# Kernel tuning notes

Measured on AMD Instinct MI355X. Metric: run time of the kernel, lower is better.

## Reference

```python
import jax, jax.numpy as jnp
import numpy as np

SPATIAL_SHAPES = ((80, 80), (40, 40), (20, 20))  # strides 8/16/32 on 640x640
NUM_HEADS = 8
N_POINTS = 4
D_MODEL = 256
OFFSET_SCALE = 0.5
N_LEVELS = len(SPATIAL_SHAPES)
TOTAL_P = N_LEVELS * N_POINTS


def setup_inputs() -> dict:
    key = jax.random.key(0)
    ks = jax.random.split(key, 11)
    B, Q = 32, 300
    S = sum(h * w for h, w in SPATIAL_SHAPES)  # 8400
    d = D_MODEL
    s = 0.02
    return {
        "hidden_states": jax.random.normal(ks[0], (B, Q, d), jnp.float32),
        "encoder_hidden_states": jax.random.normal(ks[1], (B, S, d), jnp.float32),
        "reference_points": jax.random.uniform(ks[2], (B, Q, 1, 4), jnp.float32, 0.1, 0.9),
        "W_off": jax.random.normal(ks[3], (d, NUM_HEADS * TOTAL_P * 2), jnp.float32) * s,
        "b_off": jax.random.normal(ks[4], (NUM_HEADS * TOTAL_P * 2,), jnp.float32) * s,
        "W_attn": jax.random.normal(ks[5], (d, NUM_HEADS * TOTAL_P), jnp.float32) * s,
        "b_attn": jax.random.normal(ks[6], (NUM_HEADS * TOTAL_P,), jnp.float32) * s,
        "W_val": jax.random.normal(ks[7], (d, d), jnp.float32) * s,
        "b_val": jax.random.normal(ks[8], (d,), jnp.float32) * s,
        "W_out": jax.random.normal(ks[9], (d, d), jnp.float32) * s,
        "b_out": jax.random.normal(ks[10], (d,), jnp.float32) * s,
    }


def _bilinear_sample(img, grid):
    # img: (N, H, W, C); grid: (N, Q, P, 2), normalized coords in [-1, 1]
    # torch grid_sample(mode='bilinear', padding_mode='zeros', align_corners=False)
    N, Hh, Ww, C = img.shape
    gx = (grid[..., 0] + 1.0) * (Ww * 0.5) - 0.5
    gy = (grid[..., 1] + 1.0) * (Hh * 0.5) - 0.5
    x0 = jnp.floor(gx)
    y0 = jnp.floor(gy)
    wx1 = gx - x0
    wx0 = 1.0 - wx1
    wy1 = gy - y0
    wy0 = 1.0 - wy1
    n_idx = jnp.arange(N)[:, None, None]

    def tap(ix, iy, w):
        valid = (ix >= 0) & (ix < Ww) & (iy >= 0) & (iy < Hh)
        ixc = jnp.clip(ix, 0, Ww - 1).astype(jnp.int32)
        iyc = jnp.clip(iy, 0, Hh - 1).astype(jnp.int32)
        v = img[n_idx, iyc, ixc]  # (N, Q, P, C)
        return v * (w * valid.astype(w.dtype))[..., None]

    return (tap(x0, y0, wx0 * wy0) + tap(x0 + 1.0, y0, wx1 * wy0)
            + tap(x0, y0 + 1.0, wx0 * wy1) + tap(x0 + 1.0, y0 + 1.0, wx1 * wy1))


def reference(hidden_states, encoder_hidden_states, reference_points,
              W_off, b_off, W_attn, b_attn, W_val, b_val, W_out, b_out):
    B, Q, d = hidden_states.shape
    S = encoder_hidden_states.shape[1]
    H = NUM_HEADS
    C = d // H

    value = (encoder_hidden_states @ W_val + b_val).reshape(B, S, H, C)
    offs = (hidden_states @ W_off + b_off).reshape(B, Q, H, TOTAL_P, 2)
    attn = jax.nn.softmax((hidden_states @ W_attn + b_attn).reshape(B, Q, H, TOTAL_P), axis=-1)

    # 4-d reference points branch (boxes): loc = ref_xy + off * (1/P) * ref_wh * offset_scale
    n_points_scale = jnp.full((TOTAL_P, 1), 1.0 / N_POINTS, hidden_states.dtype)
    loc = (reference_points[:, :, None, :, :2]
           + offs * n_points_scale * reference_points[:, :, None, :, 2:] * OFFSET_SCALE)
    grids = 2.0 * loc - 1.0  # method='default'
    grids = grids.transpose(0, 2, 1, 3, 4).reshape(B * H, Q, TOTAL_P, 2)

    value_bh = value.transpose(0, 2, 1, 3).reshape(B * H, S, C)

    samples = []
    start = 0
    p0 = 0
    for (h, w) in SPATIAL_SHAPES:
        v_l = value_bh[:, start:start + h * w].reshape(B * H, h, w, C)
        g_l = grids[:, :, p0:p0 + N_POINTS]
        samples.append(_bilinear_sample(v_l, g_l))
        start += h * w
        p0 += N_POINTS
    sampled = jnp.concatenate(samples, axis=2)  # (B*H, Q, TOTAL_P, C)

    attn_bh = attn.transpose(0, 2, 1, 3).reshape(B * H, Q, TOTAL_P)
    out = jnp.einsum("nqpc,nqp->nqc", sampled, attn_bh)  # (B*H, Q, C)
    out = out.reshape(B, H, Q, C).transpose(0, 2, 1, 3).reshape(B, Q, H * C)
    return out @ W_out + b_out
```

## Files before the change

kernel.cpp:

```cpp
#include <hip/hip_runtime.h>
#include <hip/hip_fp16.h>

#define DEVI __device__ __forceinline__

typedef _Float16 f16x8 __attribute__((ext_vector_type(8)));
typedef float f32x4 __attribute__((ext_vector_type(4)));

static DEVI unsigned short f2h_u(float f) {
    _Float16 h = (_Float16)f;
    return __builtin_bit_cast(unsigned short, h);
}
static DEVI float h2f_u(unsigned short u) {
    return (float)__builtin_bit_cast(_Float16, u);
}
static DEVI unsigned pk2(float a, float b) {
    return (unsigned)f2h_u(a) | ((unsigned)f2h_u(b) << 16);
}


__global__ __launch_bounds__(256) void prep_weights(
    const float* __restrict__ W_val, const float* __restrict__ W_off,
    const float* __restrict__ W_attn, const float* __restrict__ W_out,
    const float* __restrict__ b_off, const float* __restrict__ b_attn,
    unsigned short* __restrict__ Wst, unsigned short* __restrict__ Wct,
    unsigned short* __restrict__ Wot, float* __restrict__ cbias)
{
    int idx = blockIdx.x * 256 + threadIdx.x;
    if (idx < 65536) {
        int n = idx >> 8, k = idx & 255;
        Wst[(((n >> 7) * 32 + (k >> 3)) * 128 + (n & 127)) * 8 + (k & 7)] =
            f2h_u(W_val[k * 256 + n]);
    } else if (idx < 65536 + 73728) {
        int j = idx - 65536;
        int n = j >> 8, k = j & 255;
        Wct[j] = f2h_u(n < 192 ? W_off[k * 192 + n] : W_attn[k * 96 + (n - 192)]);
    } else if (idx < 204800) {
        int j = idx - 139264;
        int n = j >> 8, k = j & 255;
        Wot[j] = f2h_u(W_out[k * 256 + n]);
    } else if (idx < 205088) {
        int j = idx - 204800;
        cbias[j] = (j < 192) ? b_off[j] : b_attn[j - 192];
    }
}

__global__ __launch_bounds__(256, 2) void gemm_value(
    const float* __restrict__ A, const unsigned short* __restrict__ Wst,
    const float* __restrict__ bias, unsigned short* __restrict__ out)
{
    __shared__ __align__(16) unsigned short Bs[32 * 128 * 8];
    const int tid  = threadIdx.x;
    const int wave = tid >> 6;
    const int lane = tid & 63;
    const int l15  = lane & 15;
    const int qd   = lane >> 4;
    const size_t m0 = (size_t)blockIdx.x * 64;

#pragma unroll
    for (int it = 0; it < 16; ++it) {
        const int c = wave * 16 + it;
        const unsigned short* gp = Wst + c * 512 + lane * 8;
        unsigned short* lp = Bs + c * 512;
        __builtin_amdgcn_global_load_lds(
            (const __attribute__((address_space(1))) void*)gp,
            (__attribute__((address_space(3))) void*)lp, 16, 0, 0);
    }

    const float* arow = A + (m0 + wave * 16 + l15) * 256 + qd * 8;
    float4 a0[8], a1[8];
#pragma unroll
    for (int kt = 0; kt < 8; ++kt) {
        a0[kt] = *(const float4*)(arow + kt * 32);
        a1[kt] = *(const float4*)(arow + kt * 32 + 4);
    }
    f16x8 af[8];
#pragma unroll
    for (int kt = 0; kt < 8; ++kt) {
        union { f16x8 v; uint4 u; } t;
        t.u.x = pk2(a0[kt].x, a0[kt].y);
        t.u.y = pk2(a0[kt].z, a0[kt].w);
        t.u.z = pk2(a1[kt].x, a1[kt].y);
        t.u.w = pk2(a1[kt].z, a1[kt].w);
        af[kt] = t.v;
    }

    f32x4 acc[2][8];
#pragma unroll
    for (int h = 0; h < 2; ++h)
#pragma unroll
        for (int i = 0; i < 8; ++i) acc[h][i] = (f32x4){0.f, 0.f, 0.f, 0.f};

    __syncthreads();

#pragma unroll
    for (int kt = 0; kt < 8; ++kt) {
#pragma unroll
        for (int ni = 0; ni < 8; ++ni) {
            f16x8 bf = *(const f16x8*)&Bs[(((kt * 4 + qd) * 128) + ni * 16 + l15) * 8];
            acc[0][ni] = __builtin_amdgcn_mfma_f32_16x16x32_f16(af[kt], bf, acc[0][ni], 0, 0, 0);
        }
    }
    __syncthreads();

#pragma unroll
    for (int it = 0; it < 16; ++it) {
        const int c = wave * 16 + it;
        const unsigned short* gp = Wst + 32768 + c * 512 + lane * 8;
        unsigned short* lp = Bs + c * 512;
        __builtin_amdgcn_global_load_lds(
            (const __attribute__((address_space(1))) void*)gp,
            (__attribute__((address_space(3))) void*)lp, 16, 0, 0);
    }
    __syncthreads();
#pragma unroll
    for (int kt = 0; kt < 8; ++kt) {
#pragma unroll
        for (int ni = 0; ni < 8; ++ni) {
            f16x8 bf = *(const f16x8*)&Bs[(((kt * 4 + qd) * 128) + ni * 16 + l15) * 8];
            acc[1][ni] = __builtin_amdgcn_mfma_f32_16x16x32_f16(af[kt], bf, acc[1][ni], 0, 0, 0);
        }
    }

    constexpr int LDH = 136;
#pragma unroll
    for (int h = 0; h < 2; ++h) {
        __syncthreads();
        unsigned short* Ch = Bs;
#pragma unroll
        for (int ni = 0; ni < 8; ++ni) {
            const float bb = bias[h * 128 + ni * 16 + l15];
#pragma unroll
            for (int r = 0; r < 4; ++r) {
                Ch[(wave * 16 + qd * 4 + r) * LDH + ni * 16 + l15] =
                    f2h_u(acc[h][ni][r] + bb);
            }
        }
        __syncthreads();
        for (int f = tid; f < 64 * 16; f += 256) {
            int row = f >> 4, c8 = f & 15;
            uint4 v = *(uint4*)&Ch[row * LDH + c8 * 8];
            *(uint4*)(out + (m0 + row) * 256 + h * 128 + c8 * 8) = v;
        }
    }
}

template<int BN>
__global__ __launch_bounds__(256) void gemm_f16(
    const float* __restrict__ A, const unsigned short* __restrict__ Wt,
    const float* __restrict__ bias, float* __restrict__ outp, int ldo)
{
    constexpr int NI  = BN / 16;
    constexpr int LDA = 40;
    constexpr int LDB = 40;
    constexpr int LDC = BN + 4;
    constexpr int SM1 = 64 * LDA * 2 + BN * LDB * 2;
    constexpr int SM2 = 64 * LDC * 4;
    constexpr int SMEM = SM1 > SM2 ? SM1 : SM2;
    __shared__ __align__(16) char smem[SMEM];
    unsigned short* As = (unsigned short*)smem;
    unsigned short* Bs = (unsigned short*)(smem + 64 * LDA * 2);
    float* Cs = (float*)smem;

    const int tid  = threadIdx.x;
    const int wave = tid >> 6;
    const int lane = tid & 63;
    const int l15  = lane & 15;
    const int qd   = lane >> 4;
    const int m0   = blockIdx.y * 64;
    const int n0   = blockIdx.x * BN;

    f32x4 acc[NI];
#pragma unroll
    for (int i = 0; i < NI; i++) acc[i] = (f32x4){0.f, 0.f, 0.f, 0.f};

#pragma unroll
    for (int kt = 0; kt < 8; kt++) {
#pragma unroll
        for (int i = 0; i < 2; i++) {
            int f = tid + i * 256;
            int row = f >> 3, c4 = f & 7;
            const float4 v = *(const float4*)(A + (size_t)(m0 + row) * 256 + kt * 32 + c4 * 4);
            uint2 p;
            p.x = pk2(v.x, v.y);
            p.y = pk2(v.z, v.w);
            *(uint2*)&As[row * LDA + c4 * 4] = p;
        }
        for (int f = tid; f < BN * 4; f += 256) {
            int row = f >> 2, ch = f & 3;
            uint4 v = *(const uint4*)(Wt + (size_t)(n0 + row) * 256 + kt * 32 + ch * 8);
            *(uint4*)&Bs[row * LDB + ch * 8] = v;
        }
        __syncthreads();
        f16x8 afr = *(const f16x8*)&As[(wave * 16 + l15) * LDA + qd * 8];
#pragma unroll
        for (int ni = 0; ni < NI; ni++) {
            f16x8 fb = *(const f16x8*)&Bs[(ni * 16 + l15) * LDB + qd * 8];
            acc[ni] = __builtin_amdgcn_mfma_f32_16x16x32_f16(afr, fb, acc[ni], 0, 0, 0);
        }
        __syncthreads();
    }

#pragma unroll
    for (int ni = 0; ni < NI; ni++) {
#pragma unroll
        for (int r = 0; r < 4; r++) {
            Cs[(wave * 16 + qd * 4 + r) * LDC + ni * 16 + l15] = acc[ni][r];
        }
    }
    __syncthreads();
    for (int f = tid; f < 64 * (BN / 4); f += 256) {
        int row = f / (BN / 4), c4 = f % (BN / 4);
        float4 v = *(const float4*)&Cs[row * LDC + c4 * 4];
        const float4 bb = *(const float4*)(bias + n0 + c4 * 4);
        v.x += bb.x; v.y += bb.y; v.z += bb.z; v.w += bb.w;
        *(float4*)(outp + (size_t)(m0 + row) * ldo + n0 + c4 * 4) = v;
    }
}

__global__ __launch_bounds__(256) void sample_attn(
    const float* __restrict__ P, const float* __restrict__ refp,
    const unsigned short* __restrict__ val, float* __restrict__ out_attn)
{
    __shared__ float sP[1152];
    __shared__ float sLoc[4][8][12][3];
    const int tid   = threadIdx.x;
    const int blk   = blockIdx.x;
    const int xcd   = blk & 7;
    const int local = blk >> 3;
    const int b     = xcd + 8 * (local / 75);
    const int q0    = (local % 75) * 4;
    const int row0  = b * 300 + q0;

    {
        const float4* src = (const float4*)(P + (size_t)row0 * 288);
        for (int f = tid; f < 288; f += 256) ((float4*)sP)[f] = src[f];
    }
    __syncthreads();

    for (int j = tid; j < 384; j += 256) {
        const int r = j / 96, rem = j - r * 96;
        const int h = rem / 12, p = rem - h * 12;
        const float* Pr = sP + r * 288;
        const float* Lg = Pr + 192 + h * 12;
        float m = -1e30f;
#pragma unroll
        for (int jj = 0; jj < 12; jj++) m = fmaxf(m, Lg[jj]);
        float s = 0.f;
#pragma unroll
        for (int jj = 0; jj < 12; jj++) s += __expf(Lg[jj] - m);
        const float w = __expf(Lg[p] - m) / s;
        const float4 r4 = *(const float4*)(refp + (size_t)(row0 + r) * 4);
        sLoc[r][h][p][0] = r4.x + Pr[h * 24 + p * 2]     * 0.125f * r4.z;
        sLoc[r][h][p][1] = r4.y + Pr[h * 24 + p * 2 + 1] * 0.125f * r4.w;
        sLoc[r][h][p][2] = w;
    }
    __syncthreads();

    const int r  = tid >> 6;
    const int t6 = tid & 63;
    const int h  = t6 >> 3;
    const int l8 = t6 & 7;
    const int row = row0 + r;
    const unsigned short* vb = val + (size_t)b * 8400 * 256 + h * 32 + l8 * 4;

    float a0 = 0.f, a1 = 0.f, a2 = 0.f, a3 = 0.f;
#pragma unroll
    for (int half = 0; half < 2; ++half) {
        int   off[24];
        float kw[24];
#pragma unroll
        for (int pp = 0; pp < 6; ++pp) {
            const int p2   = half * 6 + pp;
            const int lvl  = p2 >> 2;
            const int W    = (lvl == 0) ? 80 : ((lvl == 1) ? 40 : 20);
            const int loff = (lvl == 0) ? 0 : ((lvl == 1) ? 6400 : 8000);
            const float lx = sLoc[r][h][p2][0];
            const float ly = sLoc[r][h][p2][1];
            const float w  = sLoc[r][h][p2][2];
            const float px = lx * (float)W - 0.5f;
            const float py = ly * (float)W - 0.5f;
            const float x0f = floorf(px), y0f = floorf(py);
            const float fx = px - x0f, fy = py - y0f;
            const int x0 = (int)x0f, y0 = (int)y0f;
            const int x1 = x0 + 1, y1 = y0 + 1;
            const bool vx0 = (x0 >= 0) && (x0 < W);
            const bool vx1 = (x1 >= 0) && (x1 < W);
            const bool vy0 = (y0 >= 0) && (y0 < W);
            const bool vy1 = (y1 >= 0) && (y1 < W);
            const int x0c = min(max(x0, 0), W - 1), x1c = min(max(x1, 0), W - 1);
            const int y0c = min(max(y0, 0), W - 1), y1c = min(max(y1, 0), W - 1);
            kw[pp * 4 + 0] = (vx0 && vy0) ? w * (1.f - fx) * (1.f - fy) : 0.f;
            kw[pp * 4 + 1] = (vx1 && vy0) ? w * fx * (1.f - fy) : 0.f;
            kw[pp * 4 + 2] = (vx0 && vy1) ? w * (1.f - fx) * fy : 0.f;
            kw[pp * 4 + 3] = (vx1 && vy1) ? w * fx * fy : 0.f;
            off[pp * 4 + 0] = (loff + y0c * W + x0c) * 256;
            off[pp * 4 + 1] = (loff + y0c * W + x1c) * 256;
            off[pp * 4 + 2] = (loff + y1c * W + x0c) * 256;
            off[pp * 4 + 3] = (loff + y1c * W + x1c) * 256;
        }
        uint2 u[24];
#pragma unroll
        for (int t = 0; t < 24; ++t) u[t] = *(const uint2*)(vb + off[t]);
#pragma unroll
        for (int t = 0; t < 24; ++t) {
            const float k = kw[t];
            a0 = fmaf(k, h2f_u(u[t].x & 0xffff), a0);
            a1 = fmaf(k, h2f_u(u[t].x >> 16),    a1);
            a2 = fmaf(k, h2f_u(u[t].y & 0xffff), a2);
            a3 = fmaf(k, h2f_u(u[t].y >> 16),    a3);
        }
    }
    float4 o; o.x = a0; o.y = a1; o.z = a2; o.w = a3;
    *(float4*)(out_attn + (size_t)row * 256 + h * 32 + l8 * 4) = o;
}

extern "C" void kernel_launch(void* const* d_in, const int* in_sizes, int n_in,
                              void* d_out, int out_size, void* d_ws, size_t ws_size,
                              hipStream_t stream)
{
    const float* hs     = (const float*)d_in[0];
    const float* enc    = (const float*)d_in[1];
    const float* refp   = (const float*)d_in[2];
    const float* W_off  = (const float*)d_in[3];
    const float* b_off  = (const float*)d_in[4];
    const float* W_attn = (const float*)d_in[5];
    const float* b_attn = (const float*)d_in[6];
    const float* W_val  = (const float*)d_in[7];
    const float* b_val  = (const float*)d_in[8];
    const float* W_out  = (const float*)d_in[9];
    const float* b_out  = (const float*)d_in[10];
    float* outp = (float*)d_out;

    char* ws = (char*)d_ws;
    unsigned short* val = (unsigned short*)ws;
    float* P            = (float*)(ws + 137625600);
    float* oattn        = (float*)(ws + 148684800);
    unsigned short* Wst = (unsigned short*)(ws + 158515200);
    unsigned short* Wct = (unsigned short*)(ws + 158646272);
    unsigned short* Wot = (unsigned short*)(ws + 158793728);
    float* cbias        = (float*)(ws + 158924800);

    prep_weights<<<802, 256, 0, stream>>>(W_val, W_off, W_attn, W_out,
                                          b_off, b_attn, Wst, Wct, Wot, cbias);
    gemm_f16<96><<<dim3(3, 150), 256, 0, stream>>>(hs, Wct, cbias, P, 288);
    gemm_value<<<4200, 256, 0, stream>>>(enc, Wst, b_val, val);
    sample_attn<<<2400, 256, 0, stream>>>(P, refp, val, oattn);
    gemm_f16<64><<<dim3(4, 150), 256, 0, stream>>>(oattn, Wot, b_out, outp, 256);
}
```

Measured before the change: 476.2 us.

## Merge projection GEMMs into one launch, pipeline sampling loads, fp16 attention output

```diff
diff --git a/kernel.cpp b/kernel.cpp
--- a/kernel.cpp
+++ b/kernel.cpp
@@ -44,112 +44,294 @@
     }
 }
 
-__global__ __launch_bounds__(256, 2) void gemm_value(
-    const float* __restrict__ A, const unsigned short* __restrict__ Wst,
-    const float* __restrict__ bias, unsigned short* __restrict__ out)
+__global__ __launch_bounds__(256, 2) void fused_gemms(
+    const float* __restrict__ hs, const unsigned short* __restrict__ Wct,
+    const float* __restrict__ cbias, float* __restrict__ P,
+    const float* __restrict__ enc, const unsigned short* __restrict__ Wst,
+    const float* __restrict__ bval, unsigned short* __restrict__ val)
 {
-    __shared__ __align__(16) unsigned short Bs[32 * 128 * 8];
+    __shared__ __align__(16) char smem[65536];
     const int tid  = threadIdx.x;
     const int wave = tid >> 6;
     const int lane = tid & 63;
     const int l15  = lane & 15;
     const int qd   = lane >> 4;
-    const size_t m0 = (size_t)blockIdx.x * 64;
-
-#pragma unroll
-    for (int it = 0; it < 16; ++it) {
-        const int c = wave * 16 + it;
-        const unsigned short* gp = Wst + c * 512 + lane * 8;
-        unsigned short* lp = Bs + c * 512;
-        __builtin_amdgcn_global_load_lds(
-            (const __attribute__((address_space(1))) void*)gp,
-            (__attribute__((address_space(3))) void*)lp, 16, 0, 0);
-    }
-
-    const float* arow = A + (m0 + wave * 16 + l15) * 256 + qd * 8;
-    float4 a0[8], a1[8];
-#pragma unroll
-    for (int kt = 0; kt < 8; ++kt) {
-        a0[kt] = *(const float4*)(arow + kt * 32);
-        a1[kt] = *(const float4*)(arow + kt * 32 + 4);
-    }
-    f16x8 af[8];
-#pragma unroll
-    for (int kt = 0; kt < 8; ++kt) {
-        union { f16x8 v; uint4 u; } t;
-        t.u.x = pk2(a0[kt].x, a0[kt].y);
-        t.u.y = pk2(a0[kt].z, a0[kt].w);
-        t.u.z = pk2(a1[kt].x, a1[kt].y);
-        t.u.w = pk2(a1[kt].z, a1[kt].w);
-        af[kt] = t.v;
-    }
-
-    f32x4 acc[2][8];
-#pragma unroll
-    for (int h = 0; h < 2; ++h)
-#pragma unroll
-        for (int i = 0; i < 8; ++i) acc[h][i] = (f32x4){0.f, 0.f, 0.f, 0.f};
-
+
+    if (blockIdx.x < 450) {
+        constexpr int BN  = 96;
+        constexpr int NI  = BN / 16;
+        constexpr int LDA = 40;
+        constexpr int LDB = 40;
+        constexpr int LDC = BN + 4;
+        unsigned short* As = (unsigned short*)smem;
+        unsigned short* Bs = (unsigned short*)(smem + 64 * LDA * 2);
+        float* Cs = (float*)smem;
+        const int m0 = (blockIdx.x / 3) * 64;
+        const int n0 = (blockIdx.x % 3) * BN;
+
+        f32x4 acc[NI];
+#pragma unroll
+        for (int i = 0; i < NI; i++) acc[i] = (f32x4){0.f, 0.f, 0.f, 0.f};
+
+#pragma unroll
+        for (int kt = 0; kt < 8; kt++) {
+#pragma unroll
+            for (int i = 0; i < 2; i++) {
+                int f = tid + i * 256;
+                int row = f >> 3, c4 = f & 7;
+                const float4 v = *(const float4*)(hs + (size_t)(m0 + row) * 256 + kt * 32 + c4 * 4);
+                uint2 p;
+                p.x = pk2(v.x, v.y);
+                p.y = pk2(v.z, v.w);
+                *(uint2*)&As[row * LDA + c4 * 4] = p;
+            }
+            for (int f = tid; f < BN * 4; f += 256) {
+                int row = f >> 2, ch = f & 3;
+                uint4 v = *(const uint4*)(Wct + (size_t)(n0 + row) * 256 + kt * 32 + ch * 8);
+                *(uint4*)&Bs[row * LDB + ch * 8] = v;
+            }
+            __syncthreads();
+            f16x8 afr = *(const f16x8*)&As[(wave * 16 + l15) * LDA + qd * 8];
+#pragma unroll
+            for (int ni = 0; ni < NI; ni++) {
+                f16x8 fb = *(const f16x8*)&Bs[(ni * 16 + l15) * LDB + qd * 8];
+                acc[ni] = __builtin_amdgcn_mfma_f32_16x16x32_f16(afr, fb, acc[ni], 0, 0, 0);
+            }
+            __syncthreads();
+        }
+
+#pragma unroll
+        for (int ni = 0; ni < NI; ni++) {
+#pragma unroll
+            for (int r = 0; r < 4; r++) {
+                Cs[(wave * 16 + qd * 4 + r) * LDC + ni * 16 + l15] = acc[ni][r];
+            }
+        }
+        __syncthreads();
+        for (int f = tid; f < 64 * (BN / 4); f += 256) {
+            int row = f / (BN / 4), c4 = f % (BN / 4);
+            float4 v = *(const float4*)&Cs[row * LDC + c4 * 4];
+            const float4 bb = *(const float4*)(cbias + n0 + c4 * 4);
+            v.x += bb.x; v.y += bb.y; v.z += bb.z; v.w += bb.w;
+            *(float4*)(P + (size_t)(m0 + row) * 288 + n0 + c4 * 4) = v;
+        }
+    } else {
+        unsigned short* Bs = (unsigned short*)smem;
+        const size_t m0 = (size_t)(blockIdx.x - 450) * 64;
+
+#pragma unroll
+        for (int it = 0; it < 16; ++it) {
+            const int c = wave * 16 + it;
+            const unsigned short* gp = Wst + c * 512 + lane * 8;
+            unsigned short* lp = Bs + c * 512;
+            __builtin_amdgcn_global_load_lds(
+                (const __attribute__((address_space(1))) void*)gp,
+                (__attribute__((address_space(3))) void*)lp, 16, 0, 0);
+        }
+
+        const float* arow = enc + (m0 + wave * 16 + l15) * 256 + qd * 8;
+        float4 a0[8], a1[8];
+#pragma unroll
+        for (int kt = 0; kt < 8; ++kt) {
+            a0[kt] = *(const float4*)(arow + kt * 32);
+            a1[kt] = *(const float4*)(arow + kt * 32 + 4);
+        }
+        f16x8 af[8];
+#pragma unroll
+        for (int kt = 0; kt < 8; ++kt) {
+            union { f16x8 v; uint4 u; } t;
+            t.u.x = pk2(a0[kt].x, a0[kt].y);
+            t.u.y = pk2(a0[kt].z, a0[kt].w);
+            t.u.z = pk2(a1[kt].x, a1[kt].y);
+            t.u.w = pk2(a1[kt].z, a1[kt].w);
+            af[kt] = t.v;
+        }
+
+        f32x4 acc[2][8];
+#pragma unroll
+        for (int h = 0; h < 2; ++h)
+#pragma unroll
+            for (int i = 0; i < 8; ++i) acc[h][i] = (f32x4){0.f, 0.f, 0.f, 0.f};
+
+        __syncthreads();
+
+#pragma unroll
+        for (int kt = 0; kt < 8; ++kt) {
+#pragma unroll
+            for (int ni = 0; ni < 8; ++ni) {
+                f16x8 bf = *(const f16x8*)&Bs[(((kt * 4 + qd) * 128) + ni * 16 + l15) * 8];
+                acc[0][ni] = __builtin_amdgcn_mfma_f32_16x16x32_f16(af[kt], bf, acc[0][ni], 0, 0, 0);
+            }
+        }
+        __syncthreads();
+
+#pragma unroll
+        for (int it = 0; it < 16; ++it) {
+            const int c = wave * 16 + it;
+            const unsigned short* gp = Wst + 32768 + c * 512 + lane * 8;
+            unsigned short* lp = Bs + c * 512;
+            __builtin_amdgcn_global_load_lds(
+                (const __attribute__((address_space(1))) void*)gp,
+                (__attribute__((address_space(3))) void*)lp, 16, 0, 0);
+        }
+        __syncthreads();
+#pragma unroll
+        for (int kt = 0; kt < 8; ++kt) {
+#pragma unroll
+            for (int ni = 0; ni < 8; ++ni) {
+                f16x8 bf = *(const f16x8*)&Bs[(((kt * 4 + qd) * 128) + ni * 16 + l15) * 8];
+                acc[1][ni] = __builtin_amdgcn_mfma_f32_16x16x32_f16(af[kt], bf, acc[1][ni], 0, 0, 0);
+            }
+        }
+
+        constexpr int LDH = 136;
+#pragma unroll
+        for (int h = 0; h < 2; ++h) {
+            __syncthreads();
+            unsigned short* Ch = Bs;
+#pragma unroll
+            for (int ni = 0; ni < 8; ++ni) {
+                const float bb = bval[h * 128 + ni * 16 + l15];
+#pragma unroll
+                for (int r = 0; r < 4; ++r) {
+                    Ch[(wave * 16 + qd * 4 + r) * LDH + ni * 16 + l15] =
+                        f2h_u(acc[h][ni][r] + bb);
+                }
+            }
+            __syncthreads();
+            for (int f = tid; f < 64 * 16; f += 256) {
+                int row = f >> 4, c8 = f & 15;
+                uint4 v = *(uint4*)&Ch[row * LDH + c8 * 8];
+                *(uint4*)(val + (m0 + row) * 256 + h * 128 + c8 * 8) = v;
+            }
+        }
+    }
+}
+
+__global__ __launch_bounds__(256, 4) void sample_attn(
+    const float* __restrict__ P, const float* __restrict__ refp,
+    const unsigned short* __restrict__ val, unsigned short* __restrict__ out_attn)
+{
+    __shared__ float sP[1152];
+    __shared__ float4 sLoc[4][8][12];
+    const int tid   = threadIdx.x;
+    const int blk   = blockIdx.x;
+    const int xcd   = blk & 7;
+    const int local = blk >> 3;
+    const int b     = xcd + 8 * (local / 75);
+    const int q0    = (local % 75) * 4;
+    const int row0  = b * 300 + q0;
+
+    {
+        const float4* src = (const float4*)(P + (size_t)row0 * 288);
+        for (int f = tid; f < 288; f += 256) ((float4*)sP)[f] = src[f];
+    }
     __syncthreads();
 
-#pragma unroll
-    for (int kt = 0; kt < 8; ++kt) {
-#pragma unroll
-        for (int ni = 0; ni < 8; ++ni) {
-            f16x8 bf = *(const f16x8*)&Bs[(((kt * 4 + qd) * 128) + ni * 16 + l15) * 8];
-            acc[0][ni] = __builtin_amdgcn_mfma_f32_16x16x32_f16(af[kt], bf, acc[0][ni], 0, 0, 0);
-        }
+    for (int j = tid; j < 384; j += 256) {
+        const int r = j / 96, rem = j - r * 96;
+        const int h = rem / 12, p = rem - h * 12;
+        const float* Pr = sP + r * 288;
+        const float* Lg = Pr + 192 + h * 12;
+        float m = -1e30f;
+#pragma unroll
+        for (int jj = 0; jj < 12; jj++) m = fmaxf(m, Lg[jj]);
+        float s = 0.f;
+#pragma unroll
+        for (int jj = 0; jj < 12; jj++) s += __expf(Lg[jj] - m);
+        const float w = __expf(Lg[p] - m) / s;
+        const float4 r4 = *(const float4*)(refp + (size_t)(row0 + r) * 4);
+        float4 L;
+        L.x = r4.x + Pr[h * 24 + p * 2]     * 0.125f * r4.z;
+        L.y = r4.y + Pr[h * 24 + p * 2 + 1] * 0.125f * r4.w;
+        L.z = w;
+        L.w = 0.f;
+        sLoc[r][h][p] = L;
     }
     __syncthreads();
 
-#pragma unroll
-    for (int it = 0; it < 16; ++it) {
-        const int c = wave * 16 + it;
-        const unsigned short* gp = Wst + 32768 + c * 512 + lane * 8;
-        unsigned short* lp = Bs + c * 512;
-        __builtin_amdgcn_global_load_lds(
-            (const __attribute__((address_space(1))) void*)gp,
-            (__attribute__((address_space(3))) void*)lp, 16, 0, 0);
-    }
-    __syncthreads();
-#pragma unroll
-    for (int kt = 0; kt < 8; ++kt) {
-#pragma unroll
-        for (int ni = 0; ni < 8; ++ni) {
-            f16x8 bf = *(const f16x8*)&Bs[(((kt * 4 + qd) * 128) + ni * 16 + l15) * 8];
-            acc[1][ni] = __builtin_amdgcn_mfma_f32_16x16x32_f16(af[kt], bf, acc[1][ni], 0, 0, 0);
-        }
-    }
-
-    constexpr int LDH = 136;
-#pragma unroll
-    for (int h = 0; h < 2; ++h) {
-        __syncthreads();
-        unsigned short* Ch = Bs;
-#pragma unroll
-        for (int ni = 0; ni < 8; ++ni) {
-            const float bb = bias[h * 128 + ni * 16 + l15];
-#pragma unroll
-            for (int r = 0; r < 4; ++r) {
-                Ch[(wave * 16 + qd * 4 + r) * LDH + ni * 16 + l15] =
-                    f2h_u(acc[h][ni][r] + bb);
-            }
-        }
-        __syncthreads();
-        for (int f = tid; f < 64 * 16; f += 256) {
-            int row = f >> 4, c8 = f & 15;
-            uint4 v = *(uint4*)&Ch[row * LDH + c8 * 8];
-            *(uint4*)(out + (m0 + row) * 256 + h * 128 + c8 * 8) = v;
-        }
-    }
-}
-
-template<int BN>
-__global__ __launch_bounds__(256) void gemm_f16(
-    const float* __restrict__ A, const unsigned short* __restrict__ Wt,
-    const float* __restrict__ bias, float* __restrict__ outp, int ldo)
+    const int r  = tid >> 6;
+    const int t6 = tid & 63;
+    const int h  = t6 >> 3;
+    const int l8 = t6 & 7;
+    const int row = row0 + r;
+    const unsigned short* vb = val + (size_t)b * 8400 * 256 + h * 32 + l8 * 4;
+
+    float a0 = 0.f, a1 = 0.f, a2 = 0.f, a3 = 0.f;
+
+#define ADDR(g, OFF, KW)                                                      \
+    _Pragma("unroll")                                                         \
+    for (int pp = 0; pp < 3; ++pp) {                                          \
+        const int p2   = (g) * 3 + pp;                                        \
+        const int lvl  = p2 >> 2;                                             \
+        const int W    = (lvl == 0) ? 80 : ((lvl == 1) ? 40 : 20);            \
+        const int loff = (lvl == 0) ? 0 : ((lvl == 1) ? 6400 : 8000);         \
+        const float4 L = sLoc[r][h][p2];                                      \
+        const float px = L.x * (float)W - 0.5f;                               \
+        const float py = L.y * (float)W - 0.5f;                               \
+        const float x0f = floorf(px), y0f = floorf(py);                       \
+        const float fx = px - x0f, fy = py - y0f;                             \
+        const int x0 = (int)x0f, y0 = (int)y0f;                               \
+        const int x1 = x0 + 1, y1 = y0 + 1;                                   \
+        const bool vx0 = (x0 >= 0) && (x0 < W);                               \
+        const bool vx1 = (x1 >= 0) && (x1 < W);                               \
+        const bool vy0 = (y0 >= 0) && (y0 < W);                               \
+        const bool vy1 = (y1 >= 0) && (y1 < W);                               \
+        const int x0c = min(max(x0, 0), W - 1), x1c = min(max(x1, 0), W - 1); \
+        const int y0c = min(max(y0, 0), W - 1), y1c = min(max(y1, 0), W - 1); \
+        KW[pp * 4 + 0] = (vx0 && vy0) ? L.z * (1.f - fx) * (1.f - fy) : 0.f;  \
+        KW[pp * 4 + 1] = (vx1 && vy0) ? L.z * fx * (1.f - fy) : 0.f;          \
+        KW[pp * 4 + 2] = (vx0 && vy1) ? L.z * (1.f - fx) * fy : 0.f;          \
+        KW[pp * 4 + 3] = (vx1 && vy1) ? L.z * fx * fy : 0.f;                  \
+        OFF[pp * 4 + 0] = (loff + y0c * W + x0c) * 256;                       \
+        OFF[pp * 4 + 1] = (loff + y0c * W + x1c) * 256;                       \
+        OFF[pp * 4 + 2] = (loff + y1c * W + x0c) * 256;                       \
+        OFF[pp * 4 + 3] = (loff + y1c * W + x1c) * 256;                       \
+    }
+
+#define LOADU(U, OFF)                                                         \
+    _Pragma("unroll")                                                         \
+    for (int t = 0; t < 12; ++t) U[t] = *(const uint2*)(vb + OFF[t]);
+
+#define FMAU(U, KW)                                                           \
+    _Pragma("unroll")                                                         \
+    for (int t = 0; t < 12; ++t) {                                            \
+        const float k = KW[t];                                                \
+        a0 = fmaf(k, h2f_u((unsigned short)(U[t].x & 0xffff)), a0);           \
+        a1 = fmaf(k, h2f_u((unsigned short)(U[t].x >> 16)),    a1);           \
+        a2 = fmaf(k, h2f_u((unsigned short)(U[t].y & 0xffff)), a2);           \
+        a3 = fmaf(k, h2f_u((unsigned short)(U[t].y >> 16)),    a3);           \
+    }
+
+    int   offA[12], offB[12];
+    float kwA[12], kwB[12];
+    uint2 uA[12], uB[12];
+
+    ADDR(0, offA, kwA); LOADU(uA, offA);
+    ADDR(1, offB, kwB); LOADU(uB, offB);
+    FMAU(uA, kwA);
+    ADDR(2, offA, kwA); LOADU(uA, offA);
+    FMAU(uB, kwB);
+    ADDR(3, offB, kwB); LOADU(uB, offB);
+    FMAU(uA, kwA);
+    FMAU(uB, kwB);
+
+#undef ADDR
+#undef LOADU
+#undef FMAU
+
+    uint2 o;
+    o.x = pk2(a0, a1);
+    o.y = pk2(a2, a3);
+    *(uint2*)(out_attn + (size_t)row * 256 + h * 32 + l8 * 4) = o;
+}
+
+__global__ __launch_bounds__(256) void gemm_out(
+    const unsigned short* __restrict__ A, const unsigned short* __restrict__ Wt,
+    const float* __restrict__ bias, float* __restrict__ outp)
 {
-    constexpr int NI  = BN / 16;
+    constexpr int BN  = 64;
+    constexpr int NI  = 4;
     constexpr int LDA = 40;
     constexpr int LDB = 40;
     constexpr int LDC = BN + 4;
@@ -175,18 +357,13 @@
 
 #pragma unroll
     for (int kt = 0; kt < 8; kt++) {
-#pragma unroll
-        for (int i = 0; i < 2; i++) {
-            int f = tid + i * 256;
-            int row = f >> 3, c4 = f & 7;
-            const float4 v = *(const float4*)(A + (size_t)(m0 + row) * 256 + kt * 32 + c4 * 4);
-            uint2 p;
-            p.x = pk2(v.x, v.y);
-            p.y = pk2(v.z, v.w);
-            *(uint2*)&As[row * LDA + c4 * 4] = p;
-        }
-        for (int f = tid; f < BN * 4; f += 256) {
-            int row = f >> 2, ch = f & 3;
+        {
+            int row = tid >> 2, c8 = tid & 3;
+            uint4 v = *(const uint4*)(A + (size_t)(m0 + row) * 256 + kt * 32 + c8 * 8);
+            *(uint4*)&As[row * LDA + c8 * 8] = v;
+        }
+        {
+            int row = tid >> 2, ch = tid & 3;
             uint4 v = *(const uint4*)(Wt + (size_t)(n0 + row) * 256 + kt * 32 + ch * 8);
             *(uint4*)&Bs[row * LDB + ch * 8] = v;
         }
@@ -213,105 +390,8 @@
         float4 v = *(const float4*)&Cs[row * LDC + c4 * 4];
         const float4 bb = *(const float4*)(bias + n0 + c4 * 4);
         v.x += bb.x; v.y += bb.y; v.z += bb.z; v.w += bb.w;
-        *(float4*)(outp + (size_t)(m0 + row) * ldo + n0 + c4 * 4) = v;
-    }
-}
-
-__global__ __launch_bounds__(256) void sample_attn(
-    const float* __restrict__ P, const float* __restrict__ refp,
-    const unsigned short* __restrict__ val, float* __restrict__ out_attn)
-{
-    __shared__ float sP[1152];
-    __shared__ float sLoc[4][8][12][3];
-    const int tid   = threadIdx.x;
-    const int blk   = blockIdx.x;
-    const int xcd   = blk & 7;
-    const int local = blk >> 3;
-    const int b     = xcd + 8 * (local / 75);
-    const int q0    = (local % 75) * 4;
-    const int row0  = b * 300 + q0;
-
-    {
-        const float4* src = (const float4*)(P + (size_t)row0 * 288);
-        for (int f = tid; f < 288; f += 256) ((float4*)sP)[f] = src[f];
-    }
-    __syncthreads();
-
-    for (int j = tid; j < 384; j += 256) {
-        const int r = j / 96, rem = j - r * 96;
-        const int h = rem / 12, p = rem - h * 12;
-        const float* Pr = sP + r * 288;
-        const float* Lg = Pr + 192 + h * 12;
-        float m = -1e30f;
-#pragma unroll
-        for (int jj = 0; jj < 12; jj++) m = fmaxf(m, Lg[jj]);
-        float s = 0.f;
-#pragma unroll
-        for (int jj = 0; jj < 12; jj++) s += __expf(Lg[jj] - m);
-        const float w = __expf(Lg[p] - m) / s;
-        const float4 r4 = *(const float4*)(refp + (size_t)(row0 + r) * 4);
-        sLoc[r][h][p][0] = r4.x + Pr[h * 24 + p * 2]     * 0.125f * r4.z;
-        sLoc[r][h][p][1] = r4.y + Pr[h * 24 + p * 2 + 1] * 0.125f * r4.w;
-        sLoc[r][h][p][2] = w;
-    }
-    __syncthreads();
-
-    const int r  = tid >> 6;
-    const int t6 = tid & 63;
-    const int h  = t6 >> 3;
-    const int l8 = t6 & 7;
-    const int row = row0 + r;
-    const unsigned short* vb = val + (size_t)b * 8400 * 256 + h * 32 + l8 * 4;
-
-    float a0 = 0.f, a1 = 0.f, a2 = 0.f, a3 = 0.f;
-#pragma unroll
-    for (int half = 0; half < 2; ++half) {
-        int   off[24];
-        float kw[24];
-#pragma unroll
-        for (int pp = 0; pp < 6; ++pp) {
-            const int p2   = half * 6 + pp;
-            const int lvl  = p2 >> 2;
-            const int W    = (lvl == 0) ? 80 : ((lvl == 1) ? 40 : 20);
-            const int loff = (lvl == 0) ? 0 : ((lvl == 1) ? 6400 : 8000);
-            const float lx = sLoc[r][h][p2][0];
-            const float ly = sLoc[r][h][p2][1];
-            const float w  = sLoc[r][h][p2][2];
-            const float px = lx * (float)W - 0.5f;
-            const float py = ly * (float)W - 0.5f;
-            const float x0f = floorf(px), y0f = floorf(py);
-            const float fx = px - x0f, fy = py - y0f;
-            const int x0 = (int)x0f, y0 = (int)y0f;
-            const int x1 = x0 + 1, y1 = y0 + 1;
-            const bool vx0 = (x0 >= 0) && (x0 < W);
-            const bool vx1 = (x1 >= 0) && (x1 < W);
-            const bool vy0 = (y0 >= 0) && (y0 < W);
-            const bool vy1 = (y1 >= 0) && (y1 < W);
-            const int x0c = min(max(x0, 0), W - 1), x1c = min(max(x1, 0), W - 1);
-            const int y0c = min(max(y0, 0), W - 1), y1c = min(max(y1, 0), W - 1);
-            kw[pp * 4 + 0] = (vx0 && vy0) ? w * (1.f - fx) * (1.f - fy) : 0.f;
-            kw[pp * 4 + 1] = (vx1 && vy0) ? w * fx * (1.f - fy) : 0.f;
-            kw[pp * 4 + 2] = (vx0 && vy1) ? w * (1.f - fx) * fy : 0.f;
-            kw[pp * 4 + 3] = (vx1 && vy1) ? w * fx * fy : 0.f;
-            off[pp * 4 + 0] = (loff + y0c * W + x0c) * 256;
-            off[pp * 4 + 1] = (loff + y0c * W + x1c) * 256;
-            off[pp * 4 + 2] = (loff + y1c * W + x0c) * 256;
-            off[pp * 4 + 3] = (loff + y1c * W + x1c) * 256;
-        }
-        uint2 u[24];
-#pragma unroll
-        for (int t = 0; t < 24; ++t) u[t] = *(const uint2*)(vb + off[t]);
-#pragma unroll
-        for (int t = 0; t < 24; ++t) {
-            const float k = kw[t];
-            a0 = fmaf(k, h2f_u(u[t].x & 0xffff), a0);
-            a1 = fmaf(k, h2f_u(u[t].x >> 16),    a1);
-            a2 = fmaf(k, h2f_u(u[t].y & 0xffff), a2);
-            a3 = fmaf(k, h2f_u(u[t].y >> 16),    a3);
-        }
-    }
-    float4 o; o.x = a0; o.y = a1; o.z = a2; o.w = a3;
-    *(float4*)(out_attn + (size_t)row * 256 + h * 32 + l8 * 4) = o;
+        *(float4*)(outp + (size_t)(m0 + row) * 256 + n0 + c4 * 4) = v;
+    }
 }
 
 extern "C" void kernel_launch(void* const* d_in, const int* in_sizes, int n_in,
@@ -334,16 +414,15 @@
     char* ws = (char*)d_ws;
     unsigned short* val = (unsigned short*)ws;
     float* P            = (float*)(ws + 137625600);
-    float* oattn        = (float*)(ws + 148684800);
-    unsigned short* Wst = (unsigned short*)(ws + 158515200);
-    unsigned short* Wct = (unsigned short*)(ws + 158646272);
-    unsigned short* Wot = (unsigned short*)(ws + 158793728);
-    float* cbias        = (float*)(ws + 158924800);
+    unsigned short* oat = (unsigned short*)(ws + 148684800);
+    unsigned short* Wst = (unsigned short*)(ws + 153600000);
+    unsigned short* Wct = (unsigned short*)(ws + 153731072);
+    unsigned short* Wot = (unsigned short*)(ws + 153878528);
+    float* cbias        = (float*)(ws + 154009600);
 
     prep_weights<<<802, 256, 0, stream>>>(W_val, W_off, W_attn, W_out,
                                           b_off, b_attn, Wst, Wct, Wot, cbias);
-    gemm_f16<96><<<dim3(3, 150), 256, 0, stream>>>(hs, Wct, cbias, P, 288);
-    gemm_value<<<4200, 256, 0, stream>>>(enc, Wst, b_val, val);
-    sample_attn<<<2400, 256, 0, stream>>>(P, refp, val, oattn);
-    gemm_f16<64><<<dim3(4, 150), 256, 0, stream>>>(oattn, Wot, b_out, outp, 256);
-}
+    fused_gemms<<<4650, 256, 0, stream>>>(hs, Wct, cbias, P, enc, Wst, b_val, val);
+    sample_attn<<<2400, 256, 0, stream>>>(P, refp, val, oat);
+    gemm_out<<<dim3(4, 150), 256, 0, stream>>>(oat, Wot, b_out, outp);
+}
```

Result: faster. 466.8 us (-2.0%).
